# Performance work log

Hardware: AMD Instinct MI355X
Metric: run time of the kernel (lower is better)

Reference implementation:

```python
import jax, jax.numpy as jnp
import numpy as np

N, E = 20000, 320000
CIN = 128; H = 128
EDGE_DIM = 16; SDIM = 3; KS = 3
K = KS ** SDIM          # 27 kernel weight matrices
S = 2 ** SDIM           # 8 non-zero B-spline taps per edge (degree-1)
MLP_HID = 2 * SDIM


def _glorot(key, shape, fan_in):
    return jax.random.normal(key, shape, dtype=jnp.float32) / np.sqrt(fan_in)


def setup_inputs() -> dict:
    key = jax.random.key(0)
    ks = jax.random.split(key, 16)
    inp = {
        "x": jax.random.normal(ks[0], (N, CIN), dtype=jnp.float32),
        "edge_index": jax.random.randint(ks[1], (2, E), 0, N, dtype=jnp.int64),
        "edge_attr": jax.random.normal(ks[2], (E, EDGE_DIM), dtype=jnp.float32),
        # edge preprocessor MLP
        "Wp1": _glorot(ks[3], (EDGE_DIM, MLP_HID), EDGE_DIM),
        "bp1": jnp.zeros((MLP_HID,), jnp.float32),
        "Wp2": _glorot(ks[4], (MLP_HID, SDIM), MLP_HID),
        "bp2": jnp.zeros((SDIM,), jnp.float32),
    }
    cins = [CIN, H, H]
    for l in range(3):
        inp[f"W{l}"] = _glorot(ks[5 + 3 * l], (K, cins[l], H), cins[l] * 2)
        inp[f"Wr{l}"] = _glorot(ks[6 + 3 * l], (cins[l], H), cins[l])
        inp[f"b{l}"] = jnp.zeros((H,), jnp.float32)
    return inp


def spline_basis(u):
    """Degree-1 open B-spline basis. u: [E, SDIM] in [0,1].
    Returns (weights [E,S], flat kernel indices [E,S])."""
    v = u * (KS - 1)
    lo = jnp.clip(jnp.floor(v), 0, KS - 2)
    frac = v - lo                      # [E, SDIM]
    lo = lo.astype(jnp.int32)
    ws, idxs = [], []
    for s in range(S):
        w = jnp.ones(u.shape[0], dtype=u.dtype)
        idx = jnp.zeros(u.shape[0], dtype=jnp.int32)
        stride = 1
        for d in range(SDIM):
            bit = (s >> d) & 1
            w = w * (frac[:, d] if bit else (1.0 - frac[:, d]))
            idx = idx + (lo[:, d] + bit) * stride
            stride *= KS
        ws.append(w); idxs.append(idx)
    return jnp.stack(ws, 1), jnp.stack(idxs, 1)


def spline_conv(x, src, dst, bw, bidx, W, Wr, b):
    """SplineConv with sum aggregation, root weight and bias."""
    cin = x.shape[1]
    x_src = x[src]                              # [E, Cin] gather
    T = jnp.zeros((N * K, cin), dtype=x.dtype)  # per-(node, kernel-idx) accumulator
    for s in range(S):                          # fixed small tap count
        seg = dst * K + bidx[:, s]              # [E]
        T = T + jax.ops.segment_sum(bw[:, s, None] * x_src, seg, num_segments=N * K)
    T = T.reshape(N, K, cin)
    return jnp.einsum('nki,kio->no', T, W) + x @ Wr + b


def reference(x, edge_index, edge_attr, Wp1, bp1, Wp2, bp2,
              W0, Wr0, b0, W1, Wr1, b1, W2, Wr2, b2):
    src = edge_index[0].astype(jnp.int32)
    dst = edge_index[1].astype(jnp.int32)
    # edge preprocessor MLP + sigmoid -> pseudo coords in (0,1)
    u = jax.nn.sigmoid(jax.nn.relu(edge_attr @ Wp1 + bp1) @ Wp2 + bp2)
    bw, bidx = spline_basis(u)
    h = spline_conv(x, src, dst, bw, bidx, W0, Wr0, b0)
    h = jax.nn.relu(h)  # dropout: eval mode (identity)
    h = spline_conv(h, src, dst, bw, bidx, W1, Wr1, b1)
    h = jax.nn.relu(h)
    h = spline_conv(h, src, dst, bw, bidx, W2, Wr2, b2)
    return h
```

## Files before the change

kernel.cpp:

```cpp
#include <hip/hip_runtime.h>
#include <hip/hip_bf16.h>
#include <hip/hip_fp16.h>

#define N_NODES 20000
#define E_EDGES 320000
#define CIN 128
#define HDIM 128
#define EDGE_DIM 16
#define SDIM 3
#define KS 3
#define KK 27
#define NB 28
#define KSTEPS 112
#define TLD (KK * 128)
#define WLD 28
#define MLP_HID 6

typedef __attribute__((ext_vector_type(8))) short v8s;
typedef __attribute__((ext_vector_type(4))) float v4f;
typedef unsigned short ush;

static __device__ __forceinline__ short f2bf(float v) {
    unsigned u = __float_as_uint(v);
    unsigned r = (u + 0x7fffu + ((u >> 16) & 1u)) >> 16;
    return (short)r;
}
static __device__ __forceinline__ float bf2f_lo(unsigned u) {
    return __uint_as_float(u << 16);
}
static __device__ __forceinline__ float bf2f_hi(unsigned u) {
    return __uint_as_float(u & 0xffff0000u);
}
static __device__ __forceinline__ unsigned pack2bf(float a, float b) {
    return ((unsigned)(ush)f2bf(a)) | (((unsigned)(ush)f2bf(b)) << 16);
}

__global__ void detect_kernel(const unsigned int* __restrict__ e, int* __restrict__ flag) {
    __shared__ int s_nz;
    if (threadIdx.x == 0) s_nz = 0;
    __syncthreads();
    unsigned int v = e[threadIdx.x * 2 + 1];
    if (v != 0) atomicAdd(&s_nz, 1);
    __syncthreads();
    if (threadIdx.x == 0) *flag = (s_nz > 0) ? 1 : 0;
}

__global__ void decode_edges(const void* __restrict__ eraw, const int* __restrict__ flag,
                             int* __restrict__ e32, int n) {
    int i = blockIdx.x * blockDim.x + threadIdx.x;
    if (i >= n) return;
    if (*flag) e32[i] = ((const int*)eraw)[i];
    else       e32[i] = (int)(((const long long*)eraw)[i]);
}

__global__ void edge_basis(const float* __restrict__ ea,
                           const float* __restrict__ Wp1, const float* __restrict__ bp1,
                           const float* __restrict__ Wp2, const float* __restrict__ bp2,
                           float4* __restrict__ fb) {
    __shared__ float sW1[EDGE_DIM * MLP_HID];
    __shared__ float sb1[MLP_HID];
    __shared__ float sW2[MLP_HID * SDIM];
    __shared__ float sb2[SDIM];
    int t = threadIdx.x;
    if (t < EDGE_DIM * MLP_HID) sW1[t] = Wp1[t];
    if (t < MLP_HID)            sb1[t] = bp1[t];
    if (t < MLP_HID * SDIM)     sW2[t] = Wp2[t];
    if (t < SDIM)               sb2[t] = bp2[t];
    __syncthreads();
    int e = blockIdx.x * blockDim.x + t;
    if (e >= E_EDGES) return;

    float a[EDGE_DIM];
#pragma unroll
    for (int i = 0; i < EDGE_DIM; i++) a[i] = ea[(long)e * EDGE_DIM + i];

    float hid[MLP_HID];
#pragma unroll
    for (int j = 0; j < MLP_HID; j++) {
        float s = sb1[j];
#pragma unroll
        for (int i = 0; i < EDGE_DIM; i++) s += a[i] * sW1[i * MLP_HID + j];
        hid[j] = fmaxf(s, 0.f);
    }

    float fr[SDIM];
    unsigned lp = 0;
#pragma unroll
    for (int d = 0; d < SDIM; d++) {
        float s = sb2[d];
#pragma unroll
        for (int j = 0; j < MLP_HID; j++) s += hid[j] * sW2[j * SDIM + d];
        float u = 1.f / (1.f + expf(-s));
        float v = u * (float)(KS - 1);
        float l = floorf(v);
        l = fminf(fmaxf(l, 0.f), (float)(KS - 2));
        fr[d] = v - l;
        lp |= ((unsigned)(int)l) << (8 * d);
    }
    float4 o;
    o.x = fr[0]; o.y = fr[1]; o.z = fr[2]; o.w = __uint_as_float(lp);
    fb[e] = o;
}

__global__ void zero_int(int* __restrict__ p, int n) {
    int i = blockIdx.x * blockDim.x + threadIdx.x;
    if (i < n) p[i] = 0;
}

__global__ void hist_kernel(const int* __restrict__ dst, int* __restrict__ hist) {
    int e = blockIdx.x * blockDim.x + threadIdx.x;
    if (e >= E_EDGES) return;
    atomicAdd(&hist[dst[e]], 1);
}

__global__ void scan_blk(const int* __restrict__ hist, int* __restrict__ rowptr,
                         int* __restrict__ bsum, int B) {
    __shared__ int sh[256];
    int i = blockIdx.x * 256 + threadIdx.x;
    int v = (i < B) ? hist[i] : 0;
    sh[threadIdx.x] = v;
    __syncthreads();
    for (int off = 1; off < 256; off <<= 1) {
        int t = (threadIdx.x >= off) ? sh[threadIdx.x - off] : 0;
        __syncthreads();
        sh[threadIdx.x] += t;
        __syncthreads();
    }
    if (i < B) rowptr[i] = sh[threadIdx.x] - v;
    if (threadIdx.x == 255) bsum[blockIdx.x] = sh[255];
}

__global__ void scan_top(int* __restrict__ bsum, int nb) {
    __shared__ int sh[256];
    int v = (threadIdx.x < nb) ? bsum[threadIdx.x] : 0;
    sh[threadIdx.x] = v;
    __syncthreads();
    for (int off = 1; off < 256; off <<= 1) {
        int t = (threadIdx.x >= off) ? sh[threadIdx.x - off] : 0;
        __syncthreads();
        sh[threadIdx.x] += t;
        __syncthreads();
    }
    if (threadIdx.x < nb) bsum[threadIdx.x] = sh[threadIdx.x] - v;
}

__global__ void scan_add(int* __restrict__ rowptr, const int* __restrict__ bsum, int B) {
    int i = blockIdx.x * 256 + threadIdx.x;
    if (i < B) rowptr[i] += bsum[blockIdx.x];
    if (i == 0) rowptr[B] = E_EDGES;
}

__global__ void perm_kernel(const int* __restrict__ dst,
                            const int* __restrict__ rowptr, int* __restrict__ cursor,
                            int* __restrict__ eperm) {
    int e = blockIdx.x * blockDim.x + threadIdx.x;
    if (e >= E_EDGES) return;
    int bin = dst[e];
    int pos = rowptr[bin] + atomicAdd(&cursor[bin], 1);
    eperm[pos] = e;
}

__global__ void pack_w27(const int* __restrict__ eperm, const int* __restrict__ src,
                         const float4* __restrict__ fb,
                         int* __restrict__ srcp, float* __restrict__ w28p) {
    int j = blockIdx.x * blockDim.x + threadIdx.x;
    if (j >= E_EDGES) return;
    int e = eperm[j];
    srcp[j] = src[e];
    float4 f = fb[e];
    unsigned lp = __float_as_uint(f.w);
    float fr[3] = {f.x, f.y, f.z};
    float t[3][3];
#pragma unroll
    for (int d = 0; d < 3; d++) {
        int lo = (lp >> (8 * d)) & 255;
        float fd = fr[d];
#pragma unroll
        for (int q = 0; q < 3; q++)
            t[d][q] = (q == lo) ? (1.f - fd) : (q == lo + 1) ? fd : 0.f;
    }
    float out[WLD];
#pragma unroll
    for (int k2 = 0; k2 < 3; k2++)
#pragma unroll
        for (int k1 = 0; k1 < 3; k1++)
#pragma unroll
            for (int k0 = 0; k0 < 3; k0++)
                out[k2 * 9 + k1 * 3 + k0] = t[0][k0] * t[1][k1] * t[2][k2];
    out[27] = 0.f;
    float* op = w28p + (size_t)j * WLD;
#pragma unroll
    for (int q = 0; q < WLD / 4; q++) *(float4*)(op + 4 * q) = *(float4*)(out + 4 * q);
}

__global__ void packW3_kernel(const float* __restrict__ W0, const float* __restrict__ Wr0,
                              const float* __restrict__ W1, const float* __restrict__ Wr1,
                              const float* __restrict__ W2, const float* __restrict__ Wr2,
                              short* __restrict__ hi) {
    int gid = blockIdx.x * blockDim.x + threadIdx.x;
    if (gid >= 3 * NB * 4 * 8 * 64) return;
    int lane = gid & 63;
    int nt = (gid >> 6) & 7;
    int ks = (gid >> 9) & 3;
    int kb2 = gid >> 11;
    int layer = kb2 / NB;
    int kb = kb2 - layer * NB;
    const float* W  = (layer == 0) ? W0  : (layer == 1) ? W1  : W2;
    const float* Wr = (layer == 0) ? Wr0 : (layer == 1) ? Wr1 : Wr2;
    int i0 = ks * 32 + ((lane >> 4) & 3) * 8;
    int o = nt * 16 + (lane & 15);
    const float* src = (kb < KK) ? (W + (long)kb * 16384 + (long)i0 * 128 + o)
                                 : (Wr + (long)i0 * 128 + o);
    long off = ((long)(((size_t)layer * NB + kb) * 4 + ks) * 8 + nt) * 64 * 8
             + (long)lane * 8;
#pragma unroll
    for (int j = 0; j < 8; j++) {
        float v = src[(long)j * 128];
        hi[off + j] = f2bf(v);
    }
}

__global__ void conv_xb(const float* __restrict__ x, ush* __restrict__ xb) {
    int i = blockIdx.x * blockDim.x + threadIdx.x;
    if (i >= N_NODES * CIN / 4) return;
    float4 v = ((const float4*)x)[i];
    uint2 d;
    d.x = pack2bf(v.x, v.y);
    d.y = pack2bf(v.z, v.w);
    ((uint2*)xb)[i] = d;
}

__global__ __launch_bounds__(64) void accumT_kernel(
    const ush* __restrict__ act, const int* __restrict__ rowptr,
    const int* __restrict__ srcp, const float* __restrict__ w28p,
    ush* __restrict__ T, int n0)
{
    int lane = threadIdx.x;
    int n = n0 + blockIdx.x;
    int jb = rowptr[n], je = rowptr[n + 1];

    float acc[KK][2];
#pragma unroll
    for (int k = 0; k < KK; k++) { acc[k][0] = 0.f; acc[k][1] = 0.f; }

    const ush* actl = act + lane * 2;
    const float4* w4 = (const float4*)w28p;

    if (jb < je) {
        int last = je - 1;
        unsigned xs[4];
        float4 ws[4][7];
        int sn[4];
#pragma unroll
        for (int q = 0; q < 4; q++) {
            int jq = (jb + q > last) ? last : jb + q;
            int s = srcp[jq];
            xs[q] = *(const unsigned*)(actl + (size_t)s * 128);
#pragma unroll
            for (int t = 0; t < 7; t++) ws[q][t] = w4[(size_t)jq * 7 + t];
            int jf = (jb + 4 + q > last) ? last : jb + 4 + q;
            sn[q] = srcp[jf];
        }

        for (int j = jb; j < je; j += 4) {
#pragma unroll
            for (int s = 0; s < 4; s++) {
                if (s == 0 || j + s < je) {
                    float x0 = bf2f_lo(xs[s]), x1 = bf2f_hi(xs[s]);
                    float w[28];
#pragma unroll
                    for (int t = 0; t < 7; t++) *(float4*)(w + 4 * t) = ws[s][t];
#pragma unroll
                    for (int k = 0; k < KK; k++) {
                        acc[k][0] += w[k] * x0;
                        acc[k][1] += w[k] * x1;
                    }
                }
                int jn = (j + 4 + s > last) ? last : j + 4 + s;
                xs[s] = *(const unsigned*)(actl + (size_t)sn[s] * 128);
#pragma unroll
                for (int t = 0; t < 7; t++) ws[s][t] = w4[(size_t)jn * 7 + t];
                int jf = (j + 8 + s > last) ? last : j + 8 + s;
                sn[s] = srcp[jf];
            }
        }
    }

    ush* tp = T + (size_t)(n - n0) * TLD + lane * 2;
#pragma unroll
    for (int k = 0; k < KK; k++) {
        *(unsigned*)(tp + (size_t)k * 128) = pack2bf(acc[k][0], acc[k][1]);
    }
}

__global__ __launch_bounds__(1024) void gemm2_kernel(
    const ush* __restrict__ T, const ush* __restrict__ act,
    const short* __restrict__ Wh, const float* __restrict__ bias,
    ush* __restrict__ actout, float* __restrict__ fout,
    int n0, int relu)
{
    __shared__ float S[1024][17];
    int lane = threadIdx.x & 63;
    int wave = threadIdx.x >> 6;
    int mtr = blockIdx.x;

    v4f acc[8];
#pragma unroll
    for (int nt = 0; nt < 8; nt++) acc[nt] = (v4f){0.f, 0.f, 0.f, 0.f};

    int r15 = lane & 15;
    int sub = (lane >> 4) & 3;
    int arow = mtr * 16 + r15;
    const ush* tp = T + (size_t)arow * TLD + sub * 8;
    const ush* ap = act + (size_t)(n0 + arow) * 128 + sub * 8;

    int ks0 = wave * (KSTEPS / 16);
#pragma unroll
    for (int i = 0; i < KSTEPS / 16; i++) {
        int ks = ks0 + i;
        v8s a = (ks < KK * 4) ? *(const v8s*)(tp + ks * 32)
                              : *(const v8s*)(ap + (ks - KK * 4) * 32);
        const short* wb = Wh + (size_t)ks * 4096 + (size_t)lane * 8;
#pragma unroll
        for (int nt = 0; nt < 8; nt++) {
            v8s b = *(const v8s*)(wb + (size_t)nt * 512);
            acc[nt] = __builtin_amdgcn_mfma_f32_16x16x32_bf16(a, b, acc[nt], 0, 0, 0);
        }
    }

    int r  = threadIdx.x >> 6;
    int cl = threadIdx.x & 63;
    int row = n0 + mtr * 16 + r;
#pragma unroll
    for (int p = 0; p < 2; p++) {
        __syncthreads();
#pragma unroll
        for (int q = 0; q < 16; q++)
            S[threadIdx.x][q] = acc[p * 4 + (q >> 2)][q & 3];
        __syncthreads();
        int c = p * 64 + cl;
        int ln  = (cl & 15) + 16 * (r >> 2);
        int idx = (cl >> 4) * 4 + (r & 3);
        float s = 0.f;
#pragma unroll
        for (int w = 0; w < 16; w++) s += S[w * 64 + ln][idx];
        s += bias[c];
        if (relu) s = fmaxf(s, 0.f);
        if (actout) {
            actout[(size_t)row * 128 + c] = (ush)f2bf(s);
        } else {
            fout[(size_t)row * 128 + c] = s;
        }
    }
}

extern "C" void kernel_launch(void* const* d_in, const int* in_sizes, int n_in,
                              void* d_out, int out_size, void* d_ws, size_t ws_size,
                              hipStream_t stream) {
    const float* x   = (const float*)d_in[0];
    const void*  eix = d_in[1];
    const float* ea  = (const float*)d_in[2];
    const float* Wp1 = (const float*)d_in[3];
    const float* bp1 = (const float*)d_in[4];
    const float* Wp2 = (const float*)d_in[5];
    const float* bp2 = (const float*)d_in[6];
    const float* W[3]  = {(const float*)d_in[7],  (const float*)d_in[10], (const float*)d_in[13]};
    const float* Wr[3] = {(const float*)d_in[8],  (const float*)d_in[11], (const float*)d_in[14]};
    const float* b[3]  = {(const float*)d_in[9],  (const float*)d_in[12], (const float*)d_in[15]};
    float* out = (float*)d_out;

    char* ws = (char*)d_ws;
    size_t off = 0;
    auto walloc = [&](size_t bytes) -> void* {
        void* p = ws + off;
        off = (off + bytes + 255) & ~(size_t)255;
        return p;
    };
    int*    flag    = (int*)   walloc(sizeof(int));
    int*    e32     = (int*)   walloc(sizeof(int) * 2 * E_EDGES);
    float4* fb      = (float4*)walloc(sizeof(float4) * (size_t)E_EDGES);
    int*    srcp    = (int*)   walloc(sizeof(int) * E_EDGES);
    int*    eperm   = (int*)   walloc(sizeof(int) * E_EDGES);
    float*  w28p    = (float*) walloc(sizeof(float) * (size_t)E_EDGES * WLD);
    int*    histcur = (int*)   walloc(sizeof(int) * (size_t)N_NODES * 2);
    int*    rowptr  = (int*)   walloc(sizeof(int) * (N_NODES + 1));
    int*    bsum    = (int*)   walloc(sizeof(int) * 256);
    ush*    xb      = (ush*)   walloc(sizeof(ush) * (size_t)N_NODES * 128);
    ush*    a1      = (ush*)   walloc(sizeof(ush) * (size_t)N_NODES * 128);
    ush*    a2      = (ush*)   walloc(sizeof(ush) * (size_t)N_NODES * 128);
    short*  Wh3     = (short*) walloc(sizeof(short) * (size_t)3 * NB * 128 * 128);

    int chunk_n = 10000;
    {
        const int cand[3] = {10000, 4000, 2000};
        for (int i = 0; i < 3; i++) {
            size_t need = (size_t)cand[i] * TLD * sizeof(ush);
            chunk_n = cand[i];
            if (off + need <= ws_size) break;
        }
    }
    ush* T = (ush*)walloc((size_t)chunk_n * TLD * sizeof(ush));

    int* srcv = e32;
    int* dstv = e32 + E_EDGES;
    int* hist   = histcur;
    int* cursor = histcur + N_NODES;

    detect_kernel<<<1, 1024, 0, stream>>>((const unsigned int*)eix, flag);
    decode_edges<<<(2 * E_EDGES + 255) / 256, 256, 0, stream>>>(eix, flag, e32, 2 * E_EDGES);
    edge_basis<<<(E_EDGES + 255) / 256, 256, 0, stream>>>(ea, Wp1, bp1, Wp2, bp2, fb);

    const int NBLK = (N_NODES + 255) / 256;
    zero_int<<<(N_NODES * 2 + 255) / 256, 256, 0, stream>>>(histcur, N_NODES * 2);
    hist_kernel<<<(E_EDGES + 255) / 256, 256, 0, stream>>>(dstv, hist);
    scan_blk<<<NBLK, 256, 0, stream>>>(hist, rowptr, bsum, N_NODES);
    scan_top<<<1, 256, 0, stream>>>(bsum, NBLK);
    scan_add<<<NBLK, 256, 0, stream>>>(rowptr, bsum, N_NODES);
    perm_kernel<<<(E_EDGES + 255) / 256, 256, 0, stream>>>(dstv, rowptr, cursor, eperm);
    pack_w27<<<(E_EDGES + 255) / 256, 256, 0, stream>>>(eperm, srcv, fb, srcp, w28p);

    packW3_kernel<<<(3 * NB * 4 * 8 * 64 + 255) / 256, 256, 0, stream>>>(
        W[0], Wr[0], W[1], Wr[1], W[2], Wr[2], Wh3);
    conv_xb<<<(N_NODES * CIN / 4 + 255) / 256, 256, 0, stream>>>(x, xb);

    const ush* actin = xb;
    for (int l = 0; l < 3; l++) {
        const short* Wh = Wh3 + (size_t)l * NB * 128 * 128;
        ush* actout = (l == 0) ? a1 : (l == 1) ? a2 : nullptr;
        for (int n0 = 0; n0 < N_NODES; n0 += chunk_n) {
            int cn = (n0 + chunk_n <= N_NODES) ? chunk_n : (N_NODES - n0);
            int nmt = cn / 16;
            accumT_kernel<<<cn, 64, 0, stream>>>(actin, rowptr, srcp, w28p, T, n0);
            gemm2_kernel<<<nmt, 1024, 0, stream>>>(
                T, actin, Wh, b[l], actout, (l == 2) ? out : nullptr,
                n0, (l < 2) ? 1 : 0);
        }
        if (l == 0) actin = a1; else if (l == 1) actin = a2;
    }
}
```

Measured before the change: 621.3 us.

## Pack per-edge src index and spline weights into 128-byte records staged via LDS

Merges the separate src-index array and the 28-float weight array into a single 32-float record per edge. accumT now loads 8 records per wave cooperatively with coalesced float4 loads, double-buffered in shared memory, and then issues 8 independent activation gathers at once. It also allows a single 20000-node chunk when workspace permits, which cuts the number of launches. The trade-offs are more record bytes, padded tail reads, LDS reads that broadcast to all lanes, and a larger T buffer.

```diff
diff --git a/kernel.cpp b/kernel.cpp
--- a/kernel.cpp
+++ b/kernel.cpp
@@ -13,7 +13,8 @@
 #define NB 28
 #define KSTEPS 112
 #define TLD (KK * 128)
-#define WLD 28
+#define RLD 32
+#define EPAD 8
 #define MLP_HID 6
 
 typedef __attribute__((ext_vector_type(8))) short v8s;
@@ -160,37 +161,39 @@
     eperm[pos] = e;
 }
 
-__global__ void pack_w27(const int* __restrict__ eperm, const int* __restrict__ src,
-                         const float4* __restrict__ fb,
-                         int* __restrict__ srcp, float* __restrict__ w28p) {
+__global__ void pack_rec(const int* __restrict__ eperm, const int* __restrict__ src,
+                         const float4* __restrict__ fb, float* __restrict__ rec) {
     int j = blockIdx.x * blockDim.x + threadIdx.x;
-    if (j >= E_EDGES) return;
-    int e = eperm[j];
-    srcp[j] = src[e];
-    float4 f = fb[e];
-    unsigned lp = __float_as_uint(f.w);
-    float fr[3] = {f.x, f.y, f.z};
-    float t[3][3];
-#pragma unroll
-    for (int d = 0; d < 3; d++) {
-        int lo = (lp >> (8 * d)) & 255;
-        float fd = fr[d];
-#pragma unroll
-        for (int q = 0; q < 3; q++)
-            t[d][q] = (q == lo) ? (1.f - fd) : (q == lo + 1) ? fd : 0.f;
-    }
-    float out[WLD];
-#pragma unroll
-    for (int k2 = 0; k2 < 3; k2++)
-#pragma unroll
-        for (int k1 = 0; k1 < 3; k1++)
-#pragma unroll
-            for (int k0 = 0; k0 < 3; k0++)
-                out[k2 * 9 + k1 * 3 + k0] = t[0][k0] * t[1][k1] * t[2][k2];
-    out[27] = 0.f;
-    float* op = w28p + (size_t)j * WLD;
-#pragma unroll
-    for (int q = 0; q < WLD / 4; q++) *(float4*)(op + 4 * q) = *(float4*)(out + 4 * q);
+    if (j >= E_EDGES + EPAD) return;
+    float out[RLD];
+#pragma unroll
+    for (int q = 0; q < RLD; q++) out[q] = 0.f;
+    if (j < E_EDGES) {
+        int e = eperm[j];
+        out[0] = __int_as_float(src[e]);
+        float4 f = fb[e];
+        unsigned lp = __float_as_uint(f.w);
+        float fr[3] = {f.x, f.y, f.z};
+        float t[3][3];
+#pragma unroll
+        for (int d = 0; d < 3; d++) {
+            int lo = (lp >> (8 * d)) & 255;
+            float fd = fr[d];
+#pragma unroll
+            for (int q = 0; q < 3; q++)
+                t[d][q] = (q == lo) ? (1.f - fd) : (q == lo + 1) ? fd : 0.f;
+        }
+#pragma unroll
+        for (int k2 = 0; k2 < 3; k2++)
+#pragma unroll
+            for (int k1 = 0; k1 < 3; k1++)
+#pragma unroll
+                for (int k0 = 0; k0 < 3; k0++)
+                    out[4 + k2 * 9 + k1 * 3 + k0] = t[0][k0] * t[1][k1] * t[2][k2];
+    }
+    float* op = rec + (size_t)j * RLD;
+#pragma unroll
+    for (int q = 0; q < RLD / 4; q++) *(float4*)(op + 4 * q) = *(float4*)(out + 4 * q);
 }
 
 __global__ void packW3_kernel(const float* __restrict__ W0, const float* __restrict__ Wr0,
@@ -232,56 +235,58 @@
 
 __global__ __launch_bounds__(64) void accumT_kernel(
     const ush* __restrict__ act, const int* __restrict__ rowptr,
-    const int* __restrict__ srcp, const float* __restrict__ w28p,
-    ush* __restrict__ T, int n0)
+    const float* __restrict__ rec, ush* __restrict__ T, int n0)
 {
+    __shared__ float lb[2][256];
     int lane = threadIdx.x;
     int n = n0 + blockIdx.x;
     int jb = rowptr[n], je = rowptr[n + 1];
+    int d = je - jb;
 
     float acc[KK][2];
 #pragma unroll
     for (int k = 0; k < KK; k++) { acc[k][0] = 0.f; acc[k][1] = 0.f; }
 
     const ush* actl = act + lane * 2;
-    const float4* w4 = (const float4*)w28p;
-
-    if (jb < je) {
-        int last = je - 1;
-        unsigned xs[4];
-        float4 ws[4][7];
-        int sn[4];
-#pragma unroll
-        for (int q = 0; q < 4; q++) {
-            int jq = (jb + q > last) ? last : jb + q;
-            int s = srcp[jq];
-            xs[q] = *(const unsigned*)(actl + (size_t)s * 128);
-#pragma unroll
-            for (int t = 0; t < 7; t++) ws[q][t] = w4[(size_t)jq * 7 + t];
-            int jf = (jb + 4 + q > last) ? last : jb + 4 + q;
-            sn[q] = srcp[jf];
-        }
-
-        for (int j = jb; j < je; j += 4) {
-#pragma unroll
-            for (int s = 0; s < 4; s++) {
-                if (s == 0 || j + s < je) {
-                    float x0 = bf2f_lo(xs[s]), x1 = bf2f_hi(xs[s]);
+
+    if (d > 0) {
+        int nb = (d + 7) >> 3;
+        const float4* rb = (const float4*)rec + (size_t)jb * 8;
+
+        float4 g = rb[lane];
+        *(float4*)(&lb[0][lane * 4]) = g;
+        if (nb > 1) g = rb[(size_t)64 + lane];
+
+        for (int b = 0; b < nb; ++b) {
+            int slot = b & 1;
+            if (b + 1 < nb) *(float4*)(&lb[slot ^ 1][lane * 4]) = g;
+            if (b + 2 < nb) g = rb[(size_t)(b + 2) * 64 + lane];
+
+            int sidx[8];
+#pragma unroll
+            for (int e = 0; e < 8; e++)
+                sidx[e] = __float_as_int(lb[slot][e * 32]);
+            unsigned xa[8];
+#pragma unroll
+            for (int e = 0; e < 8; e++)
+                xa[e] = *(const unsigned*)(actl + (size_t)sidx[e] * 128);
+
+            int rem = d - (b << 3);
+#pragma unroll
+            for (int e = 0; e < 8; e++) {
+                if (e < rem) {
                     float w[28];
 #pragma unroll
-                    for (int t = 0; t < 7; t++) *(float4*)(w + 4 * t) = ws[s][t];
+                    for (int q = 0; q < 7; q++)
+                        *(float4*)(w + 4 * q) =
+                            *(const float4*)(&lb[slot][e * 32 + 4 + 4 * q]);
+                    float x0 = bf2f_lo(xa[e]), x1 = bf2f_hi(xa[e]);
 #pragma unroll
                     for (int k = 0; k < KK; k++) {
                         acc[k][0] += w[k] * x0;
                         acc[k][1] += w[k] * x1;
                     }
                 }
-                int jn = (j + 4 + s > last) ? last : j + 4 + s;
-                xs[s] = *(const unsigned*)(actl + (size_t)sn[s] * 128);
-#pragma unroll
-                for (int t = 0; t < 7; t++) ws[s][t] = w4[(size_t)jn * 7 + t];
-                int jf = (j + 8 + s > last) ? last : j + 8 + s;
-                sn[s] = srcp[jf];
             }
         }
     }
@@ -379,9 +384,8 @@
     int*    flag    = (int*)   walloc(sizeof(int));
     int*    e32     = (int*)   walloc(sizeof(int) * 2 * E_EDGES);
     float4* fb      = (float4*)walloc(sizeof(float4) * (size_t)E_EDGES);
-    int*    srcp    = (int*)   walloc(sizeof(int) * E_EDGES);
     int*    eperm   = (int*)   walloc(sizeof(int) * E_EDGES);
-    float*  w28p    = (float*) walloc(sizeof(float) * (size_t)E_EDGES * WLD);
+    float*  rec     = (float*) walloc(sizeof(float) * (size_t)(E_EDGES + EPAD) * RLD);
     int*    histcur = (int*)   walloc(sizeof(int) * (size_t)N_NODES * 2);
     int*    rowptr  = (int*)   walloc(sizeof(int) * (N_NODES + 1));
     int*    bsum    = (int*)   walloc(sizeof(int) * 256);
@@ -390,10 +394,10 @@
     ush*    a2      = (ush*)   walloc(sizeof(ush) * (size_t)N_NODES * 128);
     short*  Wh3     = (short*) walloc(sizeof(short) * (size_t)3 * NB * 128 * 128);
 
-    int chunk_n = 10000;
+    int chunk_n = 2000;
     {
-        const int cand[3] = {10000, 4000, 2000};
-        for (int i = 0; i < 3; i++) {
+        const int cand[4] = {20000, 10000, 4000, 2000};
+        for (int i = 0; i < 4; i++) {
             size_t need = (size_t)cand[i] * TLD * sizeof(ush);
             chunk_n = cand[i];
             if (off + need <= ws_size) break;
@@ -417,7 +421,7 @@
     scan_top<<<1, 256, 0, stream>>>(bsum, NBLK);
     scan_add<<<NBLK, 256, 0, stream>>>(rowptr, bsum, N_NODES);
     perm_kernel<<<(E_EDGES + 255) / 256, 256, 0, stream>>>(dstv, rowptr, cursor, eperm);
-    pack_w27<<<(E_EDGES + 255) / 256, 256, 0, stream>>>(eperm, srcv, fb, srcp, w28p);
+    pack_rec<<<(E_EDGES + EPAD + 255) / 256, 256, 0, stream>>>(eperm, srcv, fb, rec);
 
     packW3_kernel<<<(3 * NB * 4 * 8 * 64 + 255) / 256, 256, 0, stream>>>(
         W[0], Wr[0], W[1], Wr[1], W[2], Wr[2], Wh3);
@@ -430,7 +434,7 @@
         for (int n0 = 0; n0 < N_NODES; n0 += chunk_n) {
             int cn = (n0 + chunk_n <= N_NODES) ? chunk_n : (N_NODES - n0);
             int nmt = cn / 16;
-            accumT_kernel<<<cn, 64, 0, stream>>>(actin, rowptr, srcp, w28p, T, n0);
+            accumT_kernel<<<cn, 64, 0, stream>>>(actin, rowptr, rec, T, n0);
             gemm2_kernel<<<nmt, 1024, 0, stream>>>(
                 T, actin, Wh, b[l], actout, (l == 2) ? out : nullptr,
                 n0, (l < 2) ? 1 : 0);
```

Result: faster. 526.8 us (-15.2%).
